# Kernel tuning notes

Measured on AMD Instinct MI355X. Metric: run time of the kernel, lower is better.

The kernel has to match this reference:

```python
import jax, jax.numpy as jnp
import numpy as np

# NF4 quantization levels (16 entries) from NF4Quantizer
NF4_LEVELS = jnp.array([
    -1.0, -0.6961928009986877, -0.5250730514526367, -0.39491748809814453,
    -0.28444138169288635, -0.18477343022823334, -0.09105003625154495, 0.0,
    0.07958029955625534, 0.16093020141124725, 0.24611230194568634,
    0.33791524171829224, 0.44070982933044434, 0.5626170039176941,
    0.7229568362236023, 1.0], dtype=jnp.float32)

OUT_F, IN_F = 4096, 4096
B, S = 2, 512

def setup_inputs() -> dict:
    key = jax.random.key(0)
    k1, k2, k3, k4, k5 = jax.random.split(key, 5)
    x = jax.random.normal(k1, (B, S, IN_F), dtype=jnp.float32)
    w0 = jax.random.normal(k2, (OUT_F, IN_F), dtype=jnp.float32) * 0.02
    nf4_idx = jax.random.randint(k3, (OUT_F, IN_F), 0, 16, dtype=jnp.int32)
    scale = jax.random.uniform(k4, (1,), dtype=jnp.float32) * 0.1 + 0.01
    zero_point = jax.random.normal(k5, (1,), dtype=jnp.float32) * 0.01
    return {"x": x, "w0": w0, "nf4_idx": nf4_idx, "scale": scale,
            "zero_point": zero_point}

def reference(x, w0, nf4_idx, scale, zero_point):
    # NF4 dequantize: look up level values, then affine (quantized*scale + zp)
    q = NF4_LEVELS[nf4_idx]                      # [out, in] float32
    deq_w = q * scale + zero_point               # dequantized adaptor weight
    # frozen base linear + dequantized low-rank-adaptor linear (QLoRA-style)
    base = jnp.einsum('bsi,oi->bso', x, w0)
    adapt = jnp.einsum('bsi,oi->bso', x, deq_w)
    return base + adapt
```

## Files before the change

### kernel.cpp

```cpp
#include <hip/hip_runtime.h>
#include <hip/hip_bf16.h>
#include <stdint.h>

#define MDIM 1024
#define NDIM 4096
#define KDIM 4096

#define BM 128
#define BN 128
#define BK 64

typedef __attribute__((ext_vector_type(4))) float f32x4;
typedef __attribute__((ext_vector_type(4))) float float4v;
typedef __attribute__((ext_vector_type(4))) int int4v;
typedef __attribute__((ext_vector_type(4))) unsigned int uint4v;
typedef __attribute__((ext_vector_type(8))) short short8;

#define GLOBAL_AS __attribute__((address_space(1)))
#define LDS_AS __attribute__((address_space(3)))

#define CFENCE asm volatile("" ::: "memory")
#define HARD_BARRIER() do {                      \
    CFENCE;                                      \
    __builtin_amdgcn_s_barrier();                \
    CFENCE;                                      \
    __builtin_amdgcn_sched_barrier(0);           \
} while (0)

__device__ __constant__ float c_nf4[16] = {
    -1.0f, -0.6961928009986877f, -0.5250730514526367f, -0.39491748809814453f,
    -0.28444138169288635f, -0.18477343022823334f, -0.09105003625154495f, 0.0f,
    0.07958029955625534f, 0.16093020141124725f, 0.24611230194568634f,
    0.33791524171829224f, 0.44070982933044434f, 0.5626170039176941f,
    0.7229568362236023f, 1.0f};

__device__ __forceinline__ unsigned bf16_rne(float f) {
    unsigned u = __float_as_uint(f);
    return (u + 0x7fffu + ((u >> 16) & 1u)) >> 16;
}

#define W_BLOCKS ((NDIM * KDIM) / (256 * 8))
#define X_BLOCKS ((MDIM * KDIM) / (256 * 8))

__global__ __launch_bounds__(256) void prep_kernel(
    const float* __restrict__ x, const float* __restrict__ w0,
    const int* __restrict__ nf4_idx, const float* __restrict__ scale_p,
    const float* __restrict__ zp_p, __hip_bfloat16* __restrict__ Wc,
    __hip_bfloat16* __restrict__ xb)
{
    const int lane = threadIdx.x & 63;
    if (blockIdx.x < W_BLOCKS) {
        const float scale = scale_p[0];
        const float zp = zp_p[0];
        const int tab = __float_as_int(c_nf4[lane & 15] * scale + zp);
        const size_t base = ((size_t)blockIdx.x * 256 + threadIdx.x) * 8;
        int4v i0 = *(const int4v*)(nf4_idx + base);
        int4v i1 = *(const int4v*)(nf4_idx + base + 4);
        float4v w_0 = *(const float4v*)(w0 + base);
        float4v w_1 = *(const float4v*)(w0 + base + 4);
        unsigned r[8];
#pragma unroll
        for (int j = 0; j < 4; j++) {
            float q = __int_as_float(__builtin_amdgcn_ds_bpermute(i0[j] * 4, tab));
            r[j] = bf16_rne(w_0[j] + q);
        }
#pragma unroll
        for (int j = 0; j < 4; j++) {
            float q = __int_as_float(__builtin_amdgcn_ds_bpermute(i1[j] * 4, tab));
            r[4 + j] = bf16_rne(w_1[j] + q);
        }
        uint4v st;
        st.x = r[0] | (r[1] << 16);
        st.y = r[2] | (r[3] << 16);
        st.z = r[4] | (r[5] << 16);
        st.w = r[6] | (r[7] << 16);
        *(uint4v*)((unsigned short*)Wc + base) = st;
    } else {
        const size_t base = ((size_t)(blockIdx.x - W_BLOCKS) * 256 + threadIdx.x) * 8;
        float4v a0 = *(const float4v*)(x + base);
        float4v a1 = *(const float4v*)(x + base + 4);
        uint4v st;
        st.x = bf16_rne(a0[0]) | (bf16_rne(a0[1]) << 16);
        st.y = bf16_rne(a0[2]) | (bf16_rne(a0[3]) << 16);
        st.z = bf16_rne(a1[0]) | (bf16_rne(a1[1]) << 16);
        st.w = bf16_rne(a1[2]) | (bf16_rne(a1[3]) << 16);
        *(uint4v*)((unsigned short*)xb + base) = st;
    }
}

__global__ __launch_bounds__(512) void gemm_kernel(
    const __hip_bfloat16* __restrict__ A,
    const __hip_bfloat16* __restrict__ B,
    float* __restrict__ C)
{
    __shared__ __hip_bfloat16 sm[3][2][BM * BK];

    const int tid = threadIdx.x;
    const int lane = tid & 63;
    const int w = tid >> 6;
    const int wr = w >> 2;
    const int wc = w & 3;

    const int bid = blockIdx.x;
    const int orig = (bid & 7) * 32 + (bid >> 3);
    const int mtile = orig & 7;
    const int ntile = orig >> 3;

    const int s_subrow = lane >> 3;
    const int s_chunkpos = lane & 7;
    int s_row[2], s_goff[2];
#pragma unroll
    for (int j = 0; j < 2; j++) {
        int row = w * 16 + j * 8 + s_subrow;
        s_row[j] = row;
        int gchunk = s_chunkpos ^ (row & 7);
        s_goff[j] = gchunk * 8;
    }

#define STAGE(buf, kt) do {                                                        \
    _Pragma("unroll")                                                              \
    for (int j = 0; j < 2; j++) {                                                  \
        const __hip_bfloat16* ga = A + (size_t)(mtile * BM + s_row[j]) * KDIM      \
                                     + (kt) * BK + s_goff[j];                      \
        __builtin_amdgcn_global_load_lds((const GLOBAL_AS void*)ga,                \
            (LDS_AS void*)&sm[buf][0][(w * 16 + j * 8) * BK], 16, 0, 0);           \
        const __hip_bfloat16* gb = B + (size_t)(ntile * BN + s_row[j]) * KDIM      \
                                     + (kt) * BK + s_goff[j];                      \
        __builtin_amdgcn_global_load_lds((const GLOBAL_AS void*)gb,                \
            (LDS_AS void*)&sm[buf][1][(w * 16 + j * 8) * BK], 16, 0, 0);           \
    }                                                                              \
} while (0)

    int a_off[2][4], b_off[2][2];
#pragma unroll
    for (int kk2 = 0; kk2 < 2; kk2++) {
#pragma unroll
        for (int m = 0; m < 4; m++) {
            int row = wr * 64 + m * 16 + (lane & 15);
            int ch = (kk2 * 4 + (lane >> 4)) ^ (row & 7);
            a_off[kk2][m] = row * BK + ch * 8;
        }
#pragma unroll
        for (int n = 0; n < 2; n++) {
            int row = wc * 32 + n * 16 + (lane & 15);
            int ch = (kk2 * 4 + (lane >> 4)) ^ (row & 7);
            b_off[kk2][n] = row * BK + ch * 8;
        }
    }

    f32x4 acc[4][2] = {};

#define COMPUTE(buf) do {                                                          \
    _Pragma("unroll")                                                              \
    for (int kk2 = 0; kk2 < 2; kk2++) {                                            \
        short8 af[4], bfv[2];                                                      \
        _Pragma("unroll")                                                          \
        for (int m = 0; m < 4; m++)                                                \
            af[m] = *(const short8*)&sm[buf][0][a_off[kk2][m]];                    \
        _Pragma("unroll")                                                          \
        for (int n = 0; n < 2; n++)                                                \
            bfv[n] = *(const short8*)&sm[buf][1][b_off[kk2][n]];                   \
        __builtin_amdgcn_s_setprio(1);                                             \
        _Pragma("unroll")                                                          \
        for (int m = 0; m < 4; m++)                                                \
            _Pragma("unroll")                                                      \
            for (int n = 0; n < 2; n++)                                            \
                acc[m][n] = __builtin_amdgcn_mfma_f32_16x16x32_bf16(               \
                    af[m], bfv[n], acc[m][n], 0, 0, 0);                            \
        __builtin_amdgcn_s_setprio(0);                                             \
    }                                                                              \
} while (0)

    const int NT = KDIM / BK;
    STAGE(0, 0);
    STAGE(1, 1);

    for (int t = 0; t < NT; t++) {
        const int cur = t % 3;
        if (t + 2 < NT) {
            STAGE((t + 2) % 3, t + 2);
            asm volatile("s_waitcnt vmcnt(8)" ::: "memory");
        } else if (t + 1 < NT) {
            asm volatile("s_waitcnt vmcnt(4)" ::: "memory");
        } else {
            asm volatile("s_waitcnt vmcnt(0)" ::: "memory");
        }
        HARD_BARRIER();
        COMPUTE(cur);
        HARD_BARRIER();
    }

    const int rbase = mtile * BM + wr * 64 + ((lane >> 4) << 2);
    const int cbase = ntile * BN + wc * 32 + (lane & 15);
#pragma unroll
    for (int m = 0; m < 4; m++) {
#pragma unroll
        for (int n = 0; n < 2; n++) {
#pragma unroll
            for (int r = 0; r < 4; r++) {
                C[(size_t)(rbase + m * 16 + r) * NDIM + cbase + n * 16] =
                    acc[m][n][r];
            }
        }
    }
#undef STAGE
#undef COMPUTE
}

__global__ void fallback_kernel(const float* __restrict__ x,
                                const float* __restrict__ w0,
                                const int* __restrict__ nf4_idx,
                                const float* __restrict__ sp,
                                const float* __restrict__ zpp,
                                float* __restrict__ out)
{
    __shared__ float As[16][16], Bs[16][17];
    const int tx = threadIdx.x, ty = threadIdx.y;
    const int n0 = blockIdx.x * 16, m0 = blockIdx.y * 16;
    const float s = sp[0], zp = zpp[0];
    float acc = 0.0f;
    for (int k0 = 0; k0 < KDIM; k0 += 16) {
        As[ty][tx] = x[(size_t)(m0 + ty) * KDIM + k0 + tx];
        int id = nf4_idx[(size_t)(n0 + ty) * KDIM + k0 + tx];
        Bs[ty][tx] = w0[(size_t)(n0 + ty) * KDIM + k0 + tx] + c_nf4[id] * s + zp;
        __syncthreads();
#pragma unroll
        for (int j = 0; j < 16; j++) acc += As[ty][j] * Bs[tx][j];
        __syncthreads();
    }
    out[(size_t)(m0 + ty) * NDIM + n0 + tx] = acc;
}

extern "C" void kernel_launch(void* const* d_in, const int* in_sizes, int n_in,
                              void* d_out, int out_size, void* d_ws, size_t ws_size,
                              hipStream_t stream) {
    const float* x = (const float*)d_in[0];
    const float* w0 = (const float*)d_in[1];
    const int* nf4_idx = (const int*)d_in[2];
    const float* scale = (const float*)d_in[3];
    const float* zp = (const float*)d_in[4];
    float* out = (float*)d_out;

    const size_t wc_bytes = (size_t)NDIM * KDIM * 2;
    const size_t xb_bytes = (size_t)MDIM * KDIM * 2;

    if (ws_size >= wc_bytes + xb_bytes) {
        __hip_bfloat16* Wc = (__hip_bfloat16*)d_ws;
        __hip_bfloat16* xb = (__hip_bfloat16*)((char*)d_ws + wc_bytes);
        prep_kernel<<<W_BLOCKS + X_BLOCKS, 256, 0, stream>>>(
            x, w0, nf4_idx, scale, zp, Wc, xb);
        gemm_kernel<<<(MDIM / BM) * (NDIM / BN), 512, 0, stream>>>(xb, Wc, out);
    } else {
        fallback_kernel<<<dim3(NDIM / 16, MDIM / 16), dim3(16, 16), 0, stream>>>(
            x, w0, nf4_idx, scale, zp, out);
    }
}
```

Measured before the change: 71.29 us.

## Split K across wave pairs with 64x64 warp tiles and LDS reduction

Each wave now computes a 64x64 output sub-tile over half of each BK=64 slice (intra-block split-K with wk), instead of a 64x32 tile over the full slice. This is meant to raise MFMA work per LDS fragment load (8 reads for 16 MFMAs per tile instead of 12 for 16). The partial sums from the two K-halves are combined through LDS after the main loop. The barrier macro also gains an explicit lgkmcnt(0) wait, and the s_setprio hints are dropped. The cost is 64 accumulator registers per thread, an extra reduction pass with a barrier, and only half the waves writing output.

```diff
diff --git a/kernel.cpp b/kernel.cpp
--- a/kernel.cpp
+++ b/kernel.cpp
@@ -19,12 +19,12 @@
 #define GLOBAL_AS __attribute__((address_space(1)))
 #define LDS_AS __attribute__((address_space(3)))
 
-#define CFENCE asm volatile("" ::: "memory")
-#define HARD_BARRIER() do {                      \
-    CFENCE;                                      \
-    __builtin_amdgcn_s_barrier();                \
-    CFENCE;                                      \
-    __builtin_amdgcn_sched_barrier(0);           \
+#define HARD_BARRIER() do {                               \
+    __builtin_amdgcn_sched_barrier(0);                    \
+    asm volatile("s_waitcnt lgkmcnt(0)" ::: "memory");    \
+    __builtin_amdgcn_s_barrier();                         \
+    asm volatile("" ::: "memory");                        \
+    __builtin_amdgcn_sched_barrier(0);                    \
 } while (0)
 
 __device__ __constant__ float c_nf4[16] = {
@@ -99,7 +99,8 @@
     const int lane = tid & 63;
     const int w = tid >> 6;
     const int wr = w >> 2;
-    const int wc = w & 3;
+    const int wc = (w >> 1) & 1;
+    const int wk = w & 1;
 
     const int bid = blockIdx.x;
     const int orig = (bid & 7) * 32 + (bid >> 3);
@@ -113,8 +114,7 @@
     for (int j = 0; j < 2; j++) {
         int row = w * 16 + j * 8 + s_subrow;
         s_row[j] = row;
-        int gchunk = s_chunkpos ^ (row & 7);
-        s_goff[j] = gchunk * 8;
+        s_goff[j] = (s_chunkpos ^ (row & 7)) * 8;
     }
 
 #define STAGE(buf, kt) do {                                                        \
@@ -131,44 +131,36 @@
     }                                                                              \
 } while (0)
 
-    int a_off[2][4], b_off[2][2];
-#pragma unroll
-    for (int kk2 = 0; kk2 < 2; kk2++) {
-#pragma unroll
-        for (int m = 0; m < 4; m++) {
-            int row = wr * 64 + m * 16 + (lane & 15);
-            int ch = (kk2 * 4 + (lane >> 4)) ^ (row & 7);
-            a_off[kk2][m] = row * BK + ch * 8;
-        }
-#pragma unroll
-        for (int n = 0; n < 2; n++) {
-            int row = wc * 32 + n * 16 + (lane & 15);
-            int ch = (kk2 * 4 + (lane >> 4)) ^ (row & 7);
-            b_off[kk2][n] = row * BK + ch * 8;
-        }
-    }
-
-    f32x4 acc[4][2] = {};
+    int a_off[4], b_off[4];
+#pragma unroll
+    for (int m = 0; m < 4; m++) {
+        int row = wr * 64 + m * 16 + (lane & 15);
+        int c = wk * 4 + (lane >> 4);
+        a_off[m] = row * BK + (c ^ (row & 7)) * 8;
+    }
+#pragma unroll
+    for (int n = 0; n < 4; n++) {
+        int row = wc * 64 + n * 16 + (lane & 15);
+        int c = wk * 4 + (lane >> 4);
+        b_off[n] = row * BK + (c ^ (row & 7)) * 8;
+    }
+
+    f32x4 acc[4][4] = {};
 
 #define COMPUTE(buf) do {                                                          \
-    _Pragma("unroll")                                                              \
-    for (int kk2 = 0; kk2 < 2; kk2++) {                                            \
-        short8 af[4], bfv[2];                                                      \
+    short8 af[4], bfv[4];                                                          \
+    _Pragma("unroll")                                                              \
+    for (int m = 0; m < 4; m++)                                                    \
+        af[m] = *(const short8*)&sm[buf][0][a_off[m]];                             \
+    _Pragma("unroll")                                                              \
+    for (int n = 0; n < 4; n++)                                                    \
+        bfv[n] = *(const short8*)&sm[buf][1][b_off[n]];                            \
+    _Pragma("unroll")                                                              \
+    for (int m = 0; m < 4; m++)                                                    \
         _Pragma("unroll")                                                          \
-        for (int m = 0; m < 4; m++)                                                \
-            af[m] = *(const short8*)&sm[buf][0][a_off[kk2][m]];                    \
-        _Pragma("unroll")                                                          \
-        for (int n = 0; n < 2; n++)                                                \
-            bfv[n] = *(const short8*)&sm[buf][1][b_off[kk2][n]];                   \
-        __builtin_amdgcn_s_setprio(1);                                             \
-        _Pragma("unroll")                                                          \
-        for (int m = 0; m < 4; m++)                                                \
-            _Pragma("unroll")                                                      \
-            for (int n = 0; n < 2; n++)                                            \
-                acc[m][n] = __builtin_amdgcn_mfma_f32_16x16x32_bf16(               \
-                    af[m], bfv[n], acc[m][n], 0, 0, 0);                            \
-        __builtin_amdgcn_s_setprio(0);                                             \
-    }                                                                              \
+        for (int n = 0; n < 4; n++)                                                \
+            acc[m][n] = __builtin_amdgcn_mfma_f32_16x16x32_bf16(                   \
+                af[m], bfv[n], acc[m][n], 0, 0, 0);                                \
 } while (0)
 
     const int NT = KDIM / BK;
@@ -190,16 +182,33 @@
         HARD_BARRIER();
     }
 
-    const int rbase = mtile * BM + wr * 64 + ((lane >> 4) << 2);
-    const int cbase = ntile * BN + wc * 32 + (lane & 15);
-#pragma unroll
-    for (int m = 0; m < 4; m++) {
-#pragma unroll
-        for (int n = 0; n < 2; n++) {
-#pragma unroll
-            for (int r = 0; r < 4; r++) {
-                C[(size_t)(rbase + m * 16 + r) * NDIM + cbase + n * 16] =
-                    acc[m][n][r];
+    float* red = (float*)&sm[0][0][0];
+    const int pair = wr * 2 + wc;
+    if (wk == 1) {
+#pragma unroll
+        for (int m = 0; m < 4; m++) {
+#pragma unroll
+            for (int n = 0; n < 4; n++) {
+                *(f32x4*)&red[pair * 4096 + (m * 4 + n) * 256 + lane * 4] =
+                    acc[m][n];
+            }
+        }
+    }
+    HARD_BARRIER();
+    if (wk == 0) {
+        const int rbase = mtile * BM + wr * 64 + ((lane >> 4) << 2);
+        const int cbase = ntile * BN + wc * 64 + (lane & 15);
+#pragma unroll
+        for (int m = 0; m < 4; m++) {
+#pragma unroll
+            for (int n = 0; n < 4; n++) {
+                f32x4 other =
+                    *(const f32x4*)&red[pair * 4096 + (m * 4 + n) * 256 + lane * 4];
+                f32x4 v = acc[m][n] + other;
+#pragma unroll
+                for (int r = 0; r < 4; r++) {
+                    C[(size_t)(rbase + m * 16 + r) * NDIM + cbase + n * 16] = v[r];
+                }
             }
         }
     }
```

Result: slower. 74.38 us (+4.3%).

## Double BK to 128 with double-buffered LDS pipeline instead of triple buffering

Applied to the files above, without the earlier changes.

Doubles the K tile to 128 so each main-loop iteration does twice the MFMA work per pair of barriers, halving the number of K iterations. The LDS ring drops from three stages to two, giving a prefetch depth of one tile, and staging and read offsets are recomputed for 16 chunks per row. The barrier now drains lgkmcnt before s_barrier, and the setprio hints around the MFMAs are removed. This trades barrier and loop overhead for less latency hiding and a larger LDS footprint per block.

```diff
diff --git a/kernel.cpp b/kernel.cpp
--- a/kernel.cpp
+++ b/kernel.cpp
@@ -8,7 +8,8 @@
 
 #define BM 128
 #define BN 128
-#define BK 64
+#define BK 128
+#define NT (KDIM / BK)
 
 typedef __attribute__((ext_vector_type(4))) float f32x4;
 typedef __attribute__((ext_vector_type(4))) float float4v;
@@ -19,12 +20,12 @@
 #define GLOBAL_AS __attribute__((address_space(1)))
 #define LDS_AS __attribute__((address_space(3)))
 
-#define CFENCE asm volatile("" ::: "memory")
-#define HARD_BARRIER() do {                      \
-    CFENCE;                                      \
-    __builtin_amdgcn_s_barrier();                \
-    CFENCE;                                      \
-    __builtin_amdgcn_sched_barrier(0);           \
+#define HARD_BARRIER() do {                               \
+    __builtin_amdgcn_sched_barrier(0);                    \
+    asm volatile("s_waitcnt lgkmcnt(0)" ::: "memory");    \
+    __builtin_amdgcn_s_barrier();                         \
+    asm volatile("" ::: "memory");                        \
+    __builtin_amdgcn_sched_barrier(0);                    \
 } while (0)
 
 __device__ __constant__ float c_nf4[16] = {
@@ -93,7 +94,7 @@
     const __hip_bfloat16* __restrict__ B,
     float* __restrict__ C)
 {
-    __shared__ __hip_bfloat16 sm[3][2][BM * BK];
+    __shared__ __hip_bfloat16 sm[2][2][BM * BK];
 
     const int tid = threadIdx.x;
     const int lane = tid & 63;
@@ -106,45 +107,44 @@
     const int mtile = orig & 7;
     const int ntile = orig >> 3;
 
-    const int s_subrow = lane >> 3;
-    const int s_chunkpos = lane & 7;
-    int s_row[2], s_goff[2];
-#pragma unroll
-    for (int j = 0; j < 2; j++) {
-        int row = w * 16 + j * 8 + s_subrow;
+    const int s_subrow = lane >> 4;
+    const int s_chunkpos = lane & 15;
+    int s_row[4], s_goff[4];
+#pragma unroll
+    for (int j = 0; j < 4; j++) {
+        int row = w * 16 + j * 4 + s_subrow;
         s_row[j] = row;
-        int gchunk = s_chunkpos ^ (row & 7);
-        s_goff[j] = gchunk * 8;
+        s_goff[j] = ((s_chunkpos ^ (row & 7)) ) * 8;
     }
 
 #define STAGE(buf, kt) do {                                                        \
     _Pragma("unroll")                                                              \
-    for (int j = 0; j < 2; j++) {                                                  \
+    for (int j = 0; j < 4; j++) {                                                  \
         const __hip_bfloat16* ga = A + (size_t)(mtile * BM + s_row[j]) * KDIM      \
                                      + (kt) * BK + s_goff[j];                      \
         __builtin_amdgcn_global_load_lds((const GLOBAL_AS void*)ga,                \
-            (LDS_AS void*)&sm[buf][0][(w * 16 + j * 8) * BK], 16, 0, 0);           \
+            (LDS_AS void*)&sm[buf][0][(w * 16 + j * 4) * BK], 16, 0, 0);           \
         const __hip_bfloat16* gb = B + (size_t)(ntile * BN + s_row[j]) * KDIM      \
                                      + (kt) * BK + s_goff[j];                      \
         __builtin_amdgcn_global_load_lds((const GLOBAL_AS void*)gb,                \
-            (LDS_AS void*)&sm[buf][1][(w * 16 + j * 8) * BK], 16, 0, 0);           \
+            (LDS_AS void*)&sm[buf][1][(w * 16 + j * 4) * BK], 16, 0, 0);           \
     }                                                                              \
 } while (0)
 
-    int a_off[2][4], b_off[2][2];
-#pragma unroll
-    for (int kk2 = 0; kk2 < 2; kk2++) {
+    int a_off[4][4], b_off[4][2];
+#pragma unroll
+    for (int kk = 0; kk < 4; kk++) {
 #pragma unroll
         for (int m = 0; m < 4; m++) {
             int row = wr * 64 + m * 16 + (lane & 15);
-            int ch = (kk2 * 4 + (lane >> 4)) ^ (row & 7);
-            a_off[kk2][m] = row * BK + ch * 8;
+            int c = kk * 4 + (lane >> 4);
+            a_off[kk][m] = row * BK + (c ^ (row & 7)) * 8;
         }
 #pragma unroll
         for (int n = 0; n < 2; n++) {
             int row = wc * 32 + n * 16 + (lane & 15);
-            int ch = (kk2 * 4 + (lane >> 4)) ^ (row & 7);
-            b_off[kk2][n] = row * BK + ch * 8;
+            int c = kk * 4 + (lane >> 4);
+            b_off[kk][n] = row * BK + (c ^ (row & 7)) * 8;
         }
     }
 
@@ -152,36 +152,30 @@
 
 #define COMPUTE(buf) do {                                                          \
     _Pragma("unroll")                                                              \
-    for (int kk2 = 0; kk2 < 2; kk2++) {                                            \
+    for (int kk = 0; kk < 4; kk++) {                                               \
         short8 af[4], bfv[2];                                                      \
         _Pragma("unroll")                                                          \
         for (int m = 0; m < 4; m++)                                                \
-            af[m] = *(const short8*)&sm[buf][0][a_off[kk2][m]];                    \
+            af[m] = *(const short8*)&sm[buf][0][a_off[kk][m]];                     \
         _Pragma("unroll")                                                          \
         for (int n = 0; n < 2; n++)                                                \
-            bfv[n] = *(const short8*)&sm[buf][1][b_off[kk2][n]];                   \
-        __builtin_amdgcn_s_setprio(1);                                             \
+            bfv[n] = *(const short8*)&sm[buf][1][b_off[kk][n]];                    \
         _Pragma("unroll")                                                          \
         for (int m = 0; m < 4; m++)                                                \
             _Pragma("unroll")                                                      \
             for (int n = 0; n < 2; n++)                                            \
                 acc[m][n] = __builtin_amdgcn_mfma_f32_16x16x32_bf16(               \
                     af[m], bfv[n], acc[m][n], 0, 0, 0);                            \
-        __builtin_amdgcn_s_setprio(0);                                             \
     }                                                                              \
 } while (0)
 
-    const int NT = KDIM / BK;
     STAGE(0, 0);
-    STAGE(1, 1);
 
     for (int t = 0; t < NT; t++) {
-        const int cur = t % 3;
-        if (t + 2 < NT) {
-            STAGE((t + 2) % 3, t + 2);
+        const int cur = t & 1;
+        if (t + 1 < NT) {
+            STAGE(cur ^ 1, t + 1);
             asm volatile("s_waitcnt vmcnt(8)" ::: "memory");
-        } else if (t + 1 < NT) {
-            asm volatile("s_waitcnt vmcnt(4)" ::: "memory");
         } else {
             asm volatile("s_waitcnt vmcnt(0)" ::: "memory");
         }
```

Result: slower. 77.25 us (+8.4%).

## Split GEMM along K into two halves with a separate reduction kernel

Applied to the files above, without the earlier changes.

Splits the K dimension in two so twice as many workgroups run, each writing an fp32 partial result to workspace, then sums the partials with a reduce kernel. The pipeline drops from triple to double buffering to cut LDS use and allow more resident blocks, and the priority hints are removed. The trade-off is extra global traffic for the partials, an additional kernel launch, and a larger workspace requirement.

```diff
diff --git a/kernel.cpp b/kernel.cpp
--- a/kernel.cpp
+++ b/kernel.cpp
@@ -9,6 +9,8 @@
 #define BM 128
 #define BN 128
 #define BK 64
+#define KSPLIT 2
+#define KHALF (KDIM / KSPLIT)
 
 typedef __attribute__((ext_vector_type(4))) float f32x4;
 typedef __attribute__((ext_vector_type(4))) float float4v;
@@ -19,12 +21,12 @@
 #define GLOBAL_AS __attribute__((address_space(1)))
 #define LDS_AS __attribute__((address_space(3)))
 
-#define CFENCE asm volatile("" ::: "memory")
-#define HARD_BARRIER() do {                      \
-    CFENCE;                                      \
-    __builtin_amdgcn_s_barrier();                \
-    CFENCE;                                      \
-    __builtin_amdgcn_sched_barrier(0);           \
+#define HARD_BARRIER() do {                               \
+    __builtin_amdgcn_sched_barrier(0);                    \
+    asm volatile("s_waitcnt lgkmcnt(0)" ::: "memory");    \
+    __builtin_amdgcn_s_barrier();                         \
+    asm volatile("" ::: "memory");                        \
+    __builtin_amdgcn_sched_barrier(0);                    \
 } while (0)
 
 __device__ __constant__ float c_nf4[16] = {
@@ -88,12 +90,12 @@
     }
 }
 
-__global__ __launch_bounds__(512) void gemm_kernel(
+__global__ __launch_bounds__(512, 4) void gemm_splitk(
     const __hip_bfloat16* __restrict__ A,
     const __hip_bfloat16* __restrict__ B,
-    float* __restrict__ C)
-{
-    __shared__ __hip_bfloat16 sm[3][2][BM * BK];
+    float* __restrict__ Cp)
+{
+    __shared__ __hip_bfloat16 sm[2][2][BM * BK];
 
     const int tid = threadIdx.x;
     const int lane = tid & 63;
@@ -102,6 +104,134 @@
     const int wc = w & 3;
 
     const int bid = blockIdx.x;
+    const int orig = (bid & 7) * 64 + (bid >> 3);
+    const int ks = orig & 1;
+    const int tile = orig >> 1;
+    const int mtile = tile & 7;
+    const int ntile = tile >> 3;
+    const int kbase = ks * KHALF;
+
+    const int s_subrow = lane >> 3;
+    const int s_chunkpos = lane & 7;
+    int s_row[2], s_goff[2];
+#pragma unroll
+    for (int j = 0; j < 2; j++) {
+        int row = w * 16 + j * 8 + s_subrow;
+        s_row[j] = row;
+        s_goff[j] = (s_chunkpos ^ (row & 7)) * 8;
+    }
+
+#define STAGE(buf, kt) do {                                                        \
+    _Pragma("unroll")                                                              \
+    for (int j = 0; j < 2; j++) {                                                  \
+        const __hip_bfloat16* ga = A + (size_t)(mtile * BM + s_row[j]) * KDIM      \
+                                     + kbase + (kt) * BK + s_goff[j];              \
+        __builtin_amdgcn_global_load_lds((const GLOBAL_AS void*)ga,                \
+            (LDS_AS void*)&sm[buf][0][(w * 16 + j * 8) * BK], 16, 0, 0);           \
+        const __hip_bfloat16* gb = B + (size_t)(ntile * BN + s_row[j]) * KDIM      \
+                                     + kbase + (kt) * BK + s_goff[j];              \
+        __builtin_amdgcn_global_load_lds((const GLOBAL_AS void*)gb,                \
+            (LDS_AS void*)&sm[buf][1][(w * 16 + j * 8) * BK], 16, 0, 0);           \
+    }                                                                              \
+} while (0)
+
+    int a_off[2][4], b_off[2][2];
+#pragma unroll
+    for (int kk2 = 0; kk2 < 2; kk2++) {
+#pragma unroll
+        for (int m = 0; m < 4; m++) {
+            int row = wr * 64 + m * 16 + (lane & 15);
+            int ch = (kk2 * 4 + (lane >> 4)) ^ (row & 7);
+            a_off[kk2][m] = row * BK + ch * 8;
+        }
+#pragma unroll
+        for (int n = 0; n < 2; n++) {
+            int row = wc * 32 + n * 16 + (lane & 15);
+            int ch = (kk2 * 4 + (lane >> 4)) ^ (row & 7);
+            b_off[kk2][n] = row * BK + ch * 8;
+        }
+    }
+
+    f32x4 acc[4][2] = {};
+
+#define COMPUTE(buf) do {                                                          \
+    _Pragma("unroll")                                                              \
+    for (int kk2 = 0; kk2 < 2; kk2++) {                                            \
+        short8 af[4], bfv[2];                                                      \
+        _Pragma("unroll")                                                          \
+        for (int m = 0; m < 4; m++)                                                \
+            af[m] = *(const short8*)&sm[buf][0][a_off[kk2][m]];                    \
+        _Pragma("unroll")                                                          \
+        for (int n = 0; n < 2; n++)                                                \
+            bfv[n] = *(const short8*)&sm[buf][1][b_off[kk2][n]];                   \
+        _Pragma("unroll")                                                          \
+        for (int m = 0; m < 4; m++)                                                \
+            _Pragma("unroll")                                                      \
+            for (int n = 0; n < 2; n++)                                            \
+                acc[m][n] = __builtin_amdgcn_mfma_f32_16x16x32_bf16(               \
+                    af[m], bfv[n], acc[m][n], 0, 0, 0);                            \
+    }                                                                              \
+} while (0)
+
+    const int NT = KHALF / BK;
+    STAGE(0, 0);
+
+    for (int t = 0; t < NT; t++) {
+        const int cur = t & 1;
+        if (t + 1 < NT) {
+            STAGE(cur ^ 1, t + 1);
+            asm volatile("s_waitcnt vmcnt(4)" ::: "memory");
+        } else {
+            asm volatile("s_waitcnt vmcnt(0)" ::: "memory");
+        }
+        HARD_BARRIER();
+        COMPUTE(cur);
+        HARD_BARRIER();
+    }
+
+    float* Cout = Cp + (size_t)ks * MDIM * NDIM;
+    const int rbase = mtile * BM + wr * 64 + ((lane >> 4) << 2);
+    const int cbase = ntile * BN + wc * 32 + (lane & 15);
+#pragma unroll
+    for (int m = 0; m < 4; m++) {
+#pragma unroll
+        for (int n = 0; n < 2; n++) {
+#pragma unroll
+            for (int r = 0; r < 4; r++) {
+                Cout[(size_t)(rbase + m * 16 + r) * NDIM + cbase + n * 16] =
+                    acc[m][n][r];
+            }
+        }
+    }
+#undef STAGE
+#undef COMPUTE
+}
+
+#define R_BLOCKS ((MDIM * NDIM) / (256 * 4))
+
+__global__ __launch_bounds__(256) void reduce_kernel(
+    const float* __restrict__ Cp, float* __restrict__ C)
+{
+    const size_t base = ((size_t)blockIdx.x * 256 + threadIdx.x) * 4;
+    float4v a = *(const float4v*)(Cp + base);
+    float4v b = *(const float4v*)(Cp + (size_t)MDIM * NDIM + base);
+    *(float4v*)(C + base) = a + b;
+}
+
+__global__ __launch_bounds__(512) void gemm_single(
+    const __hip_bfloat16* __restrict__ A,
+    const __hip_bfloat16* __restrict__ B,
+    float* __restrict__ C)
+{
+    __shared__ __hip_bfloat16 sm[3][2][BM * BK];
+
+    const int tid = threadIdx.x;
+    const int lane = tid & 63;
+    const int w = tid >> 6;
+    const int wr = w >> 2;
+    const int wc = w & 3;
+
+    const int bid = blockIdx.x;
     const int orig = (bid & 7) * 32 + (bid >> 3);
     const int mtile = orig & 7;
     const int ntile = orig >> 3;
@@ -113,8 +243,7 @@
     for (int j = 0; j < 2; j++) {
         int row = w * 16 + j * 8 + s_subrow;
         s_row[j] = row;
-        int gchunk = s_chunkpos ^ (row & 7);
-        s_goff[j] = gchunk * 8;
+        s_goff[j] = (s_chunkpos ^ (row & 7)) * 8;
     }
 
 #define STAGE(buf, kt) do {                                                        \
@@ -160,14 +289,12 @@
         _Pragma("unroll")                                                          \
         for (int n = 0; n < 2; n++)                                                \
             bfv[n] = *(const short8*)&sm[buf][1][b_off[kk2][n]];                   \
-        __builtin_amdgcn_s_setprio(1);                                             \
         _Pragma("unroll")                                                          \
         for (int m = 0; m < 4; m++)                                                \
             _Pragma("unroll")                                                      \
             for (int n = 0; n < 2; n++)                                            \
                 acc[m][n] = __builtin_amdgcn_mfma_f32_16x16x32_bf16(               \
                     af[m], bfv[n], acc[m][n], 0, 0, 0);                            \
-        __builtin_amdgcn_s_setprio(0);                                             \
     }                                                                              \
 } while (0)
 
@@ -243,13 +370,23 @@
 
     const size_t wc_bytes = (size_t)NDIM * KDIM * 2;
     const size_t xb_bytes = (size_t)MDIM * KDIM * 2;
-
-    if (ws_size >= wc_bytes + xb_bytes) {
+    const size_t cp_bytes = (size_t)KSPLIT * MDIM * NDIM * 4;
+
+    if (ws_size >= wc_bytes + xb_bytes + cp_bytes) {
+        __hip_bfloat16* Wc = (__hip_bfloat16*)d_ws;
+        __hip_bfloat16* xb = (__hip_bfloat16*)((char*)d_ws + wc_bytes);
+        float* Cp = (float*)((char*)d_ws + wc_bytes + xb_bytes);
+        prep_kernel<<<W_BLOCKS + X_BLOCKS, 256, 0, stream>>>(
+            x, w0, nf4_idx, scale, zp, Wc, xb);
+        gemm_splitk<<<(MDIM / BM) * (NDIM / BN) * KSPLIT, 512, 0, stream>>>(
+            xb, Wc, Cp);
+        reduce_kernel<<<R_BLOCKS, 256, 0, stream>>>(Cp, out);
+    } else if (ws_size >= wc_bytes + xb_bytes) {
         __hip_bfloat16* Wc = (__hip_bfloat16*)d_ws;
         __hip_bfloat16* xb = (__hip_bfloat16*)((char*)d_ws + wc_bytes);
         prep_kernel<<<W_BLOCKS + X_BLOCKS, 256, 0, stream>>>(
             x, w0, nf4_idx, scale, zp, Wc, xb);
-        gemm_kernel<<<(MDIM / BM) * (NDIM / BN), 512, 0, stream>>>(xb, Wc, out);
+        gemm_single<<<(MDIM / BM) * (NDIM / BN), 512, 0, stream>>>(xb, Wc, out);
     } else {
         fallback_kernel<<<dim3(NDIM / 16, MDIM / 16), dim3(16, 16), 0, stream>>>(
             x, w0, nf4_idx, scale, zp, out);
```

Result: slower. 75.48 us (+5.9%).
